# Optimization experiments

Hardware: AMD Instinct MI355X
Metric: run time of the kernel (lower is better)

The kernel has to match this reference:

```python
import jax, jax.numpy as jnp
import numpy as np

INPUT_SIZE = 512
HIDDEN_SIZE = 1024
BATCH = 16384


def setup_inputs() -> dict:
    key = jax.random.key(0)
    ks = jax.random.split(key, 11)
    s_x = 1.0 / np.sqrt(INPUT_SIZE)
    s_h = 1.0 / np.sqrt(HIDDEN_SIZE)
    inp = {
        "x": jax.random.normal(ks[0], (BATCH, INPUT_SIZE), dtype=jnp.float32),
        "hidden": jax.random.normal(ks[1], (BATCH, HIDDEN_SIZE), dtype=jnp.float32),
        # Linear weights stored as (in, out) for x @ W
        "Wxr": jax.random.uniform(ks[2], (INPUT_SIZE, HIDDEN_SIZE), jnp.float32, -s_x, s_x),
        "bxr": jax.random.uniform(ks[3], (HIDDEN_SIZE,), jnp.float32, -s_x, s_x),
        "Whr": jax.random.uniform(ks[4], (HIDDEN_SIZE, HIDDEN_SIZE), jnp.float32, -s_h, s_h),
        "Wxz": jax.random.uniform(ks[5], (INPUT_SIZE, HIDDEN_SIZE), jnp.float32, -s_x, s_x),
        "bxz": jax.random.uniform(ks[6], (HIDDEN_SIZE,), jnp.float32, -s_x, s_x),
        "Whz": jax.random.uniform(ks[7], (HIDDEN_SIZE, HIDDEN_SIZE), jnp.float32, -s_h, s_h),
        "Wxh": jax.random.uniform(ks[8], (INPUT_SIZE, HIDDEN_SIZE), jnp.float32, -s_x, s_x),
        "bxh": jax.random.uniform(ks[9], (HIDDEN_SIZE,), jnp.float32, -s_x, s_x),
        "Whh": jax.random.uniform(ks[10], (HIDDEN_SIZE, HIDDEN_SIZE), jnp.float32, -s_h, s_h),
    }
    return inp


def reference(x, hidden, Wxr, bxr, Whr, Wxz, bxz, Whz, Wxh, bxh, Whh):
    # GRU cell, single timestep.
    r = jax.nn.sigmoid(x @ Wxr + bxr + hidden @ Whr)          # reset gate (B,H)
    z = jax.nn.sigmoid(x @ Wxz + bxz + hidden @ Whz)          # update gate (B,H)
    h_cand = jnp.tanh(x @ Wxh + bxh + (r * hidden) @ Whh)     # candidate (B,H)
    return z * hidden + (1.0 - z) * h_cand
```

## Files before the change

### kernel.cpp

```cpp
#include <hip/hip_runtime.h>

typedef unsigned short u16;
typedef unsigned int u32;
typedef __bf16 bf16x8 __attribute__((ext_vector_type(8)));
typedef float f32x4 __attribute__((ext_vector_type(4)));

#define B_ROWS 16384
#define K1 1536

__device__ __forceinline__ u16 f2bf(float f) {
  u32 u = __float_as_uint(f);
  u = (u + 0x7fffu + ((u >> 16) & 1u)) >> 16;
  return (u16)u;
}
__device__ __forceinline__ float bf2f(u16 b) {
  return __uint_as_float(((u32)b) << 16);
}
__device__ __forceinline__ void gload_lds16(const void* g, void* l) {
  __builtin_amdgcn_global_load_lds((const __attribute__((address_space(1))) void*)g,
                                   (__attribute__((address_space(3))) void*)l,
                                   16, 0, 0);
}

__global__ void prep(const float* __restrict__ x, const float* __restrict__ h,
                     u16* __restrict__ xh,
                     const float* __restrict__ Wxr, const float* __restrict__ Whr,
                     const float* __restrict__ Wxz, const float* __restrict__ Whz,
                     const float* __restrict__ Wxh, const float* __restrict__ Whh,
                     u16* __restrict__ W1t, u16* __restrict__ W2t) {
  if (blockIdx.x < 24576) {
    const int iv = blockIdx.x * 256 + threadIdx.x;
    const int row = iv / 384;
    const int col = (iv - row * 384) * 4;
    const float* src = (col < 512) ? x + (size_t)row * 512 + col
                                   : h + (size_t)row * 1024 + (col - 512);
    float4 v = *(const float4*)src;
    u32 a = (u32)f2bf(v.x) | ((u32)f2bf(v.y) << 16);
    u32 b = (u32)f2bf(v.z) | ((u32)f2bf(v.w) << 16);
    *(uint2*)(xh + (size_t)row * 1536 + col) = make_uint2(a, b);
    return;
  }
  __shared__ float tile[32][33];
  const int idx2 = blockIdx.x - 24576;
  const int z = idx2 >> 10;
  const int rem = idx2 & 1023;
  const int by = rem >> 5, bx = rem & 31;
  const float* W;
  u16* T;
  int Ks, koff, roff;
  switch (z) {
    case 0:  W = Wxr; T = W1t; Ks = 512;  koff = 0;   roff = 0;    break;
    case 1:  W = Whr; T = W1t; Ks = 1024; koff = 512; roff = 0;    break;
    case 2:  W = Wxz; T = W1t; Ks = 512;  koff = 0;   roff = 1024; break;
    case 3:  W = Whz; T = W1t; Ks = 1024; koff = 512; roff = 1024; break;
    case 4:  W = Wxh; T = W2t; Ks = 512;  koff = 0;   roff = 0;    break;
    default: W = Whh; T = W2t; Ks = 1024; koff = 512; roff = 0;    break;
  }
  if (by * 32 >= Ks) return;
  const int tx = threadIdx.x & 31, ty = threadIdx.x >> 5;
#pragma unroll
  for (int r = 0; r < 32; r += 8)
    tile[ty + r][tx] = W[(size_t)(by * 32 + ty + r) * 1024 + bx * 32 + tx];
  __syncthreads();
#pragma unroll
  for (int r = 0; r < 32; r += 8)
    T[(size_t)(roff + bx * 32 + ty + r) * K1 + koff + by * 32 + tx] = f2bf(tile[tx][ty + r]);
}

struct Src {
  const u16 *A, *B;
  u32 sA, sB;
};

__device__ __forceinline__ void gemm256(const Src& S, int nt, int brow, int bcol,
                                        u16* AsU, u16* BsU, f32x4 acc[8][4]) {
  const int tid = threadIdx.x;
  const int l = tid & 63;
  const int wid = tid >> 6;
  const int wr = wid >> 2, wc = wid & 3;
  const int lr = l & 15, kq = l >> 4;
  const int swzB = (lr & 7) * 16;
  const int kswzE = ((tid & 7) ^ ((tid >> 3) & 7)) * 8;
  const int r = tid >> 3;
  char* AsB = (char*)AsU;
  char* BsB = (char*)BsU;
  const int ldsQ = wid << 10;
  const int colK0 = (kq * 16) ^ swzB;
  const int colK1 = (64 + kq * 16) ^ swzB;
  int aRow[8], bRow[4];
#pragma unroll
  for (int m = 0; m < 8; ++m) aRow[m] = (wr * 128 + m * 16 + lr) * 128;
#pragma unroll
  for (int n = 0; n < 4; ++n) bRow[n] = (wc * 64 + n * 16 + lr) * 128;

  u32 offA[4], offB[4];
#pragma unroll
  for (int q = 0; q < 4; ++q) {
    offA[q] = (u32)((brow + q * 64 + r) * S.sA + kswzE) * 2u;
    offB[q] = (u32)((bcol + q * 64 + r) * S.sB + kswzE) * 2u;
  }

#define STG_A01(q_, c_) gload_lds16((const char*)S.A + offA[q_], \
    AsB + (c_) * 32768 + (q_) * 8192 + ldsQ)
#define STG_A23(q_, c_) gload_lds16((const char*)S.A + offA[q_], \
    AsB + (c_) * 32768 + 16384 + ((q_) - 2) * 8192 + ldsQ)
#define STG_B(q_, c_)   gload_lds16((const char*)S.B + offB[q_], \
    BsB + (c_) * 32768 + ((q_) >> 1) * 16384 + ((q_) & 1) * 8192 + ldsQ)

  STG_A01(0, 0); STG_A01(1, 0);
  STG_A23(2, 0); STG_A23(3, 0);
  STG_B(0, 0); STG_B(1, 0); STG_B(2, 0); STG_B(3, 0);
  offA[0] += 128; offA[1] += 128;
  STG_A01(0, 1); STG_A01(1, 1);
  offA[0] += 128; offA[1] += 128;
  offA[2] += 128; offA[3] += 128;
  offB[0] += 128; offB[1] += 128; offB[2] += 128; offB[3] += 128;
  asm volatile("s_waitcnt vmcnt(2)" ::: "memory");
  __builtin_amdgcn_s_barrier();
  asm volatile("" ::: "memory");

  for (int t = 0; t < nt; ++t) {
    const int c = t & 1;
    const int cb = c << 15;
    bf16x8 a[4][2], b[4][2];
#pragma unroll
    for (int m = 0; m < 4; ++m) {
      a[m][0] = *(const bf16x8*)(AsB + cb + aRow[m] + colK0);
      a[m][1] = *(const bf16x8*)(AsB + cb + aRow[m] + colK1);
    }
#pragma unroll
    for (int n = 0; n < 2; ++n) {
      b[n][0] = *(const bf16x8*)(BsB + cb + bRow[n] + colK0);
      b[n][1] = *(const bf16x8*)(BsB + cb + bRow[n] + colK1);
    }
    if (t + 1 < nt) { STG_A23(2, c ^ 1); STG_A23(3, c ^ 1); }
    asm volatile("s_waitcnt lgkmcnt(8)" ::: "memory");
    __builtin_amdgcn_s_barrier();
    asm volatile("s_waitcnt lgkmcnt(0)" ::: "memory");
    __builtin_amdgcn_sched_barrier(0);
    __builtin_amdgcn_s_setprio(1);
#pragma unroll
    for (int kk = 0; kk < 2; ++kk)
#pragma unroll
      for (int m = 0; m < 4; ++m)
#pragma unroll
        for (int n = 0; n < 2; ++n)
          acc[m][n] = __builtin_amdgcn_mfma_f32_16x16x32_bf16(a[m][kk], b[n][kk], acc[m][n], 0, 0, 0);
    __builtin_amdgcn_s_setprio(0);
    __builtin_amdgcn_s_barrier();
    asm volatile("" ::: "memory");
#pragma unroll
    for (int n = 2; n < 4; ++n) {
      b[n][0] = *(const bf16x8*)(BsB + cb + bRow[n] + colK0);
      b[n][1] = *(const bf16x8*)(BsB + cb + bRow[n] + colK1);
    }
    if (t + 1 < nt) { STG_B(0, c ^ 1); STG_B(1, c ^ 1); }
    __builtin_amdgcn_s_barrier();
    asm volatile("s_waitcnt lgkmcnt(0)" ::: "memory");
    __builtin_amdgcn_sched_barrier(0);
    __builtin_amdgcn_s_setprio(1);
#pragma unroll
    for (int kk = 0; kk < 2; ++kk)
#pragma unroll
      for (int m = 0; m < 4; ++m)
#pragma unroll
        for (int n = 2; n < 4; ++n)
          acc[m][n] = __builtin_amdgcn_mfma_f32_16x16x32_bf16(a[m][kk], b[n][kk], acc[m][n], 0, 0, 0);
    __builtin_amdgcn_s_setprio(0);
    __builtin_amdgcn_s_barrier();
    asm volatile("" ::: "memory");
#pragma unroll
    for (int m = 0; m < 4; ++m) {
      a[m][0] = *(const bf16x8*)(AsB + cb + aRow[m + 4] + colK0);
      a[m][1] = *(const bf16x8*)(AsB + cb + aRow[m + 4] + colK1);
    }
    if (t + 1 < nt) { STG_B(2, c ^ 1); STG_B(3, c ^ 1); }
    __builtin_amdgcn_s_barrier();
    asm volatile("s_waitcnt lgkmcnt(0)" ::: "memory");
    __builtin_amdgcn_sched_barrier(0);
    __builtin_amdgcn_s_setprio(1);
#pragma unroll
    for (int kk = 0; kk < 2; ++kk)
#pragma unroll
      for (int m = 0; m < 4; ++m)
#pragma unroll
        for (int n = 2; n < 4; ++n)
          acc[m + 4][n] = __builtin_amdgcn_mfma_f32_16x16x32_bf16(a[m][kk], b[n][kk], acc[m + 4][n], 0, 0, 0);
    __builtin_amdgcn_s_setprio(0);
    __builtin_amdgcn_s_barrier();
    asm volatile("" ::: "memory");
    if (t + 2 < nt) { STG_A01(0, c); STG_A01(1, c); }
    __builtin_amdgcn_s_barrier();
    __builtin_amdgcn_s_setprio(1);
#pragma unroll
    for (int kk = 0; kk < 2; ++kk)
#pragma unroll
      for (int m = 0; m < 4; ++m)
#pragma unroll
        for (int n = 0; n < 2; ++n)
          acc[m + 4][n] = __builtin_amdgcn_mfma_f32_16x16x32_bf16(a[m][kk], b[n][kk], acc[m + 4][n], 0, 0, 0);
    __builtin_amdgcn_s_setprio(0);
    if (t + 2 < nt) { asm volatile("s_waitcnt vmcnt(2)" ::: "memory"); }
    else            { asm volatile("s_waitcnt vmcnt(0)" ::: "memory"); }
    __builtin_amdgcn_s_barrier();
    asm volatile("" ::: "memory");
    offA[0] += 128; offA[1] += 128; offA[2] += 128; offA[3] += 128;
    offB[0] += 128; offB[1] += 128; offB[2] += 128; offB[3] += 128;
  }
#undef STG_A01
#undef STG_A23
#undef STG_B
}

__global__ __launch_bounds__(512, 1) void gru_gemm1(
    const u16* __restrict__ xh, const u16* __restrict__ W1t,
    const float* __restrict__ bxr, const float* __restrict__ bxz,
    u16* __restrict__ rhb, u16* __restrict__ zb) {
  __shared__ __align__(16) u16 As[2 * 256 * 64];
  __shared__ __align__(16) u16 Bs[2 * 256 * 64];
  const int orig = blockIdx.x;
  const int slot = orig >> 3;
  const int mt = (orig & 7) + 8 * (slot >> 3);
  const int jt = slot & 7;
  const int brow = mt * 256;
  const int jcol = jt * 256;

  Src S { xh, W1t, K1, K1 };
  f32x4 acc[8][4] = {};
  gemm256(S, 24, brow, jcol, As, Bs, acc);

  const int l = threadIdx.x & 63;
  const int wid = threadIdx.x >> 6;
  const int wr = wid >> 2, wc = wid & 3;
  const int colb = jcol + wc * 64 + (l & 15);
  const int rowb = brow + wr * 128 + (l >> 4) * 4;
  if (jt < 4) {
#pragma unroll
    for (int n = 0; n < 4; ++n) {
      const int col = colb + n * 16;
      const float bias = bxr[col];
#pragma unroll
      for (int m = 0; m < 8; ++m)
#pragma unroll
        for (int j = 0; j < 4; ++j) {
          const int row = rowb + m * 16 + j;
          const float rg = 1.f / (1.f + __expf(-(acc[m][n][j] + bias)));
          const float hv = bf2f(xh[(size_t)row * K1 + 512 + col]);
          rhb[(size_t)row * 1024 + col] = f2bf(rg * hv);
        }
    }
  } else {
#pragma unroll
    for (int n = 0; n < 4; ++n) {
      const int col = colb + n * 16 - 1024;
      const float bias = bxz[col];
#pragma unroll
      for (int m = 0; m < 8; ++m)
#pragma unroll
        for (int j = 0; j < 4; ++j) {
          const int row = rowb + m * 16 + j;
          const float zg = 1.f / (1.f + __expf(-(acc[m][n][j] + bias)));
          zb[(size_t)row * 1024 + col] = f2bf(zg);
        }
    }
  }
}

__global__ __launch_bounds__(512, 1) void gru_gemm2(
    const u16* __restrict__ xh, const u16* __restrict__ rhb,
    const u16* __restrict__ W2t, const float* __restrict__ bxh,
    const u16* __restrict__ zb, float* __restrict__ out) {
  __shared__ __align__(16) u16 As[2 * 256 * 64];
  __shared__ __align__(16) u16 Bs[2 * 128 * 64];
  const int orig = blockIdx.x;
  const int wg = (orig & 7) * 64 + (orig >> 3);
  const int mt = wg & 63;
  const int jt = wg >> 6;
  const int brow = mt * 256;
  const int jcol = jt * 128;

  const int tid = threadIdx.x;
  const int l = tid & 63;
  const int wid = tid >> 6;
  const int wrk = wid >> 1, wc = wid & 1;
  const int lr = l & 15, kq = l >> 4;
  const int swzB = (lr & 7) * 16;
  const int kswzE = ((tid & 7) ^ ((tid >> 3) & 7)) * 8;
  const int r = tid >> 3;
  char* AsB = (char*)As;
  char* BsB = (char*)Bs;
  const int ldsQ = wid << 10;
  const int colK0 = (kq * 16) ^ swzB;
  const int colK1 = (64 + kq * 16) ^ swzB;
  int aRow[4], bRow[4];
#pragma unroll
  for (int m = 0; m < 4; ++m) aRow[m] = (wrk * 64 + m * 16 + lr) * 128;
#pragma unroll
  for (int n = 0; n < 4; ++n) bRow[n] = (wc * 64 + n * 16 + lr) * 128;

  const u16* pA01 = xh;
  const u16* pA23 = xh;
  u32 offA[4], offB[2];
#pragma unroll
  for (int q = 0; q < 4; ++q) offA[q] = (u32)((brow + q * 64 + r) * K1 + kswzE) * 2u;
#pragma unroll
  for (int q = 0; q < 2; ++q) offB[q] = (u32)((jcol + q * 64 + r) * K1 + kswzE) * 2u;

#define G2_A01(q_, c_) gload_lds16((const char*)pA01 + offA[q_], \
    AsB + (c_) * 32768 + (q_) * 8192 + ldsQ)
#define G2_A23(q_, c_) gload_lds16((const char*)pA23 + offA[q_], \
    AsB + (c_) * 32768 + 16384 + ((q_) - 2) * 8192 + ldsQ)
#define G2_B(q_, c_)   gload_lds16((const char*)W2t + offB[q_], \
    BsB + (c_) * 16384 + (q_) * 8192 + ldsQ)

  G2_A01(0, 0); G2_A01(1, 0);
  G2_A23(2, 0); G2_A23(3, 0);
  G2_B(0, 0); G2_B(1, 0);
  offA[0] += 128; offA[1] += 128;
  G2_A01(0, 1); G2_A01(1, 1);
  offA[0] += 128; offA[1] += 128;
  offA[2] += 128; offA[3] += 128;
  offB[0] += 128; offB[1] += 128;
  asm volatile("s_waitcnt vmcnt(2)" ::: "memory");
  __builtin_amdgcn_s_barrier();
  asm volatile("" ::: "memory");

  f32x4 acc[4][4] = {};
  const int nt = 24;
  for (int t = 0; t < nt; ++t) {
    const int c = t & 1;
    const int cbA = c << 15;
    const int cbB = c << 14;
    bf16x8 a01[2][2], a23[2][2], b01[2][2], b23[2][2];
#pragma unroll
    for (int m = 0; m < 2; ++m) {
      a01[m][0] = *(const bf16x8*)(AsB + cbA + aRow[m] + colK0);
      a01[m][1] = *(const bf16x8*)(AsB + cbA + aRow[m] + colK1);
    }
#pragma unroll
    for (int n = 0; n < 2; ++n) {
      b01[n][0] = *(const bf16x8*)(BsB + cbB + bRow[n] + colK0);
      b01[n][1] = *(const bf16x8*)(BsB + cbB + bRow[n] + colK1);
    }
    if (t + 1 < nt) { G2_A23(2, c ^ 1); G2_A23(3, c ^ 1); }
    __builtin_amdgcn_s_barrier();
    asm volatile("s_waitcnt lgkmcnt(0)" ::: "memory");
    __builtin_amdgcn_sched_barrier(0);
    __builtin_amdgcn_s_setprio(1);
#pragma unroll
    for (int kk = 0; kk < 2; ++kk)
#pragma unroll
      for (int m = 0; m < 2; ++m)
#pragma unroll
        for (int n = 0; n < 2; ++n)
          acc[m][n] = __builtin_amdgcn_mfma_f32_16x16x32_bf16(a01[m][kk], b01[n][kk], acc[m][n], 0, 0, 0);
    __builtin_amdgcn_s_setprio(0);
    __builtin_amdgcn_s_barrier();
    asm volatile("" ::: "memory");
#pragma unroll
    for (int n = 0; n < 2; ++n) {
      b23[n][0] = *(const bf16x8*)(BsB + cbB + bRow[n + 2] + colK0);
      b23[n][1] = *(const bf16x8*)(BsB + cbB + bRow[n + 2] + colK1);
    }
    if (t + 1 < nt) { G2_B(0, c ^ 1); G2_B(1, c ^ 1); }
    __builtin_amdgcn_s_barrier();
    asm volatile("s_waitcnt lgkmcnt(0)" ::: "memory");
    __builtin_amdgcn_sched_barrier(0);
    __builtin_amdgcn_s_setprio(1);
#pragma unroll
    for (int kk = 0; kk < 2; ++kk)
#pragma unroll
      for (int m = 0; m < 2; ++m)
#pragma unroll
        for (int n = 0; n < 2; ++n)
          acc[m][n + 2] = __builtin_amdgcn_mfma_f32_16x16x32_bf16(a01[m][kk], b23[n][kk], acc[m][n + 2], 0, 0, 0);
    __builtin_amdgcn_s_setprio(0);
    __builtin_amdgcn_s_barrier();
    asm volatile("" ::: "memory");
#pragma unroll
    for (int m = 0; m < 2; ++m) {
      a23[m][0] = *(const bf16x8*)(AsB + cbA + aRow[m + 2] + colK0);
      a23[m][1] = *(const bf16x8*)(AsB + cbA + aRow[m + 2] + colK1);
    }
    __builtin_amdgcn_s_barrier();
    asm volatile("s_waitcnt lgkmcnt(0)" ::: "memory");
    __builtin_amdgcn_sched_barrier(0);
    __builtin_amdgcn_s_setprio(1);
#pragma unroll
    for (int kk = 0; kk < 2; ++kk)
#pragma unroll
      for (int m = 0; m < 2; ++m)
#pragma unroll
        for (int n = 0; n < 2; ++n)
          acc[m + 2][n + 2] = __builtin_amdgcn_mfma_f32_16x16x32_bf16(a23[m][kk], b23[n][kk], acc[m + 2][n + 2], 0, 0, 0);
    __builtin_amdgcn_s_setprio(0);
    __builtin_amdgcn_s_barrier();
    asm volatile("" ::: "memory");
    if (t + 2 < nt) { G2_A01(0, c); G2_A01(1, c); }
    __builtin_amdgcn_s_barrier();
    __builtin_amdgcn_s_setprio(1);
#pragma unroll
    for (int kk = 0; kk < 2; ++kk)
#pragma unroll
      for (int m = 0; m < 2; ++m)
#pragma unroll
        for (int n = 0; n < 2; ++n)
          acc[m + 2][n] = __builtin_amdgcn_mfma_f32_16x16x32_bf16(a23[m][kk], b01[n][kk], acc[m + 2][n], 0, 0, 0);
    __builtin_amdgcn_s_setprio(0);
    if (t + 2 < nt) { asm volatile("s_waitcnt vmcnt(2)" ::: "memory"); }
    else            { asm volatile("s_waitcnt vmcnt(0)" ::: "memory"); }
    __builtin_amdgcn_s_barrier();
    asm volatile("" ::: "memory");
    if (t == 5) {
      pA01 = rhb;
      offA[0] = (u32)((brow + 0 * 64 + r) * 1024 + kswzE) * 2u;
      offA[1] = (u32)((brow + 1 * 64 + r) * 1024 + kswzE) * 2u;
    } else { offA[0] += 128; offA[1] += 128; }
    if (t == 6) {
      pA23 = rhb;
      offA[2] = (u32)((brow + 2 * 64 + r) * 1024 + kswzE) * 2u;
      offA[3] = (u32)((brow + 3 * 64 + r) * 1024 + kswzE) * 2u;
    } else { offA[2] += 128; offA[3] += 128; }
    offB[0] += 128; offB[1] += 128;
  }
#undef G2_A01
#undef G2_A23
#undef G2_B

  const int colb = jcol + wc * 64 + (l & 15);
  const int rowb = brow + wrk * 64 + (l >> 4) * 4;
#pragma unroll
  for (int n = 0; n < 4; ++n) {
    const int col = colb + n * 16;
    const float bias = bxh[col];
#pragma unroll
    for (int m = 0; m < 4; ++m)
#pragma unroll
      for (int j = 0; j < 4; ++j) {
        const int row = rowb + m * 16 + j;
        const size_t idx = (size_t)row * 1024 + col;
        const float e = __expf(2.f * (acc[m][n][j] + bias));
        const float hc = 1.f - 2.f / (e + 1.f);
        const float z = bf2f(zb[idx]);
        const float h = bf2f(xh[(size_t)row * K1 + 512 + col]);
        out[idx] = z * h + (1.f - z) * hc;
      }
  }
}

extern "C" void kernel_launch(void* const* d_in, const int* in_sizes, int n_in,
                              void* d_out, int out_size, void* d_ws, size_t ws_size,
                              hipStream_t stream) {
  const float* x      = (const float*)d_in[0];
  const float* hidden = (const float*)d_in[1];
  const float* Wxr = (const float*)d_in[2];
  const float* bxr = (const float*)d_in[3];
  const float* Whr = (const float*)d_in[4];
  const float* Wxz = (const float*)d_in[5];
  const float* bxz = (const float*)d_in[6];
  const float* Whz = (const float*)d_in[7];
  const float* Wxh = (const float*)d_in[8];
  const float* bxh = (const float*)d_in[9];
  const float* Whh = (const float*)d_in[10];
  float* out = (float*)d_out;
  (void)in_sizes; (void)n_in; (void)out_size; (void)ws_size;

  char* p = (char*)d_ws;
  u16* xh  = (u16*)p; p += (size_t)B_ROWS * K1 * 2;
  u16* W1t = (u16*)p; p += (size_t)2048 * K1 * 2;
  u16* W2t = (u16*)p; p += (size_t)1024 * K1 * 2;
  u16* rhb = (u16*)p; p += (size_t)B_ROWS * 1024 * 2;
  u16* zb  = (u16*)p; p += (size_t)B_ROWS * 1024 * 2;

  prep<<<24576 + 6144, 256, 0, stream>>>(x, hidden, xh,
                                         Wxr, Whr, Wxz, Whz, Wxh, Whh, W1t, W2t);
  gru_gemm1<<<512, 512, 0, stream>>>(xh, W1t, bxr, bxz, rhb, zb);
  gru_gemm2<<<512, 512, 0, stream>>>(xh, rhb, W2t, bxh, zb, out);
}
```

Before: 251.5 us.

## Replace gemm1's pipelined 256x256 tile with simple single-buffered 128x128 tiles

Rewrites the first GEMM kernel from a 256x256, 512-thread, double-buffered, finely interleaved pipeline into a 128x128, 256-thread kernel with a single LDS buffer and a K-step of 32. It launches 2048 blocks with two blocks per CU, relying on occupancy rather than explicit prefetch to hide memory latency. The cost is more global traffic per FLOP from the smaller tiles and no overlap of loads with MFMA inside a block. This looks like a simplification or probe that could easily lose to the tuned pipeline.

```diff
diff --git a/kernel.cpp b/kernel.cpp
--- a/kernel.cpp
+++ b/kernel.cpp
@@ -67,180 +67,80 @@
     T[(size_t)(roff + bx * 32 + ty + r) * K1 + koff + by * 32 + tx] = f2bf(tile[tx][ty + r]);
 }
 
-struct Src {
-  const u16 *A, *B;
-  u32 sA, sB;
-};
-
-__device__ __forceinline__ void gemm256(const Src& S, int nt, int brow, int bcol,
-                                        u16* AsU, u16* BsU, f32x4 acc[8][4]) {
+__global__ __launch_bounds__(256, 2) void gru_gemm1(
+    const u16* __restrict__ xh, const u16* __restrict__ W1t,
+    const float* __restrict__ bxr, const float* __restrict__ bxz,
+    u16* __restrict__ rhb, u16* __restrict__ zb) {
+  __shared__ __align__(16) u16 As[128 * 32];
+  __shared__ __align__(16) u16 Bs[128 * 32];
+  const int orig = blockIdx.x;
+  const int slot = orig >> 3;
+  const int jt = slot & 15;
+  const int mt = (orig & 7) + 8 * (slot >> 4);
+  const int brow = mt * 128;
+  const int bcol = jt * 128;
+
   const int tid = threadIdx.x;
   const int l = tid & 63;
   const int wid = tid >> 6;
-  const int wr = wid >> 2, wc = wid & 3;
+  const int wrq = wid >> 1, wcq = wid & 1;
   const int lr = l & 15, kq = l >> 4;
-  const int swzB = (lr & 7) * 16;
-  const int kswzE = ((tid & 7) ^ ((tid >> 3) & 7)) * 8;
-  const int r = tid >> 3;
-  char* AsB = (char*)AsU;
-  char* BsB = (char*)BsU;
-  const int ldsQ = wid << 10;
-  const int colK0 = (kq * 16) ^ swzB;
-  const int colK1 = (64 + kq * 16) ^ swzB;
-  int aRow[8], bRow[4];
-#pragma unroll
-  for (int m = 0; m < 8; ++m) aRow[m] = (wr * 128 + m * 16 + lr) * 128;
-#pragma unroll
-  for (int n = 0; n < 4; ++n) bRow[n] = (wc * 64 + n * 16 + lr) * 128;
-
-  u32 offA[4], offB[4];
-#pragma unroll
-  for (int q = 0; q < 4; ++q) {
-    offA[q] = (u32)((brow + q * 64 + r) * S.sA + kswzE) * 2u;
-    offB[q] = (u32)((bcol + q * 64 + r) * S.sB + kswzE) * 2u;
-  }
-
-#define STG_A01(q_, c_) gload_lds16((const char*)S.A + offA[q_], \
-    AsB + (c_) * 32768 + (q_) * 8192 + ldsQ)
-#define STG_A23(q_, c_) gload_lds16((const char*)S.A + offA[q_], \
-    AsB + (c_) * 32768 + 16384 + ((q_) - 2) * 8192 + ldsQ)
-#define STG_B(q_, c_)   gload_lds16((const char*)S.B + offB[q_], \
-    BsB + (c_) * 32768 + ((q_) >> 1) * 16384 + ((q_) & 1) * 8192 + ldsQ)
-
-  STG_A01(0, 0); STG_A01(1, 0);
-  STG_A23(2, 0); STG_A23(3, 0);
-  STG_B(0, 0); STG_B(1, 0); STG_B(2, 0); STG_B(3, 0);
-  offA[0] += 128; offA[1] += 128;
-  STG_A01(0, 1); STG_A01(1, 1);
-  offA[0] += 128; offA[1] += 128;
-  offA[2] += 128; offA[3] += 128;
-  offB[0] += 128; offB[1] += 128; offB[2] += 128; offB[3] += 128;
-  asm volatile("s_waitcnt vmcnt(2)" ::: "memory");
-  __builtin_amdgcn_s_barrier();
-  asm volatile("" ::: "memory");
-
-  for (int t = 0; t < nt; ++t) {
-    const int c = t & 1;
-    const int cb = c << 15;
-    bf16x8 a[4][2], b[4][2];
-#pragma unroll
-    for (int m = 0; m < 4; ++m) {
-      a[m][0] = *(const bf16x8*)(AsB + cb + aRow[m] + colK0);
-      a[m][1] = *(const bf16x8*)(AsB + cb + aRow[m] + colK1);
-    }
-#pragma unroll
-    for (int n = 0; n < 2; ++n) {
-      b[n][0] = *(const bf16x8*)(BsB + cb + bRow[n] + colK0);
-      b[n][1] = *(const bf16x8*)(BsB + cb + bRow[n] + colK1);
-    }
-    if (t + 1 < nt) { STG_A23(2, c ^ 1); STG_A23(3, c ^ 1); }
-    asm volatile("s_waitcnt lgkmcnt(8)" ::: "memory");
-    __builtin_amdgcn_s_barrier();
+  const int colK = (kq * 16) ^ ((lr & 3) * 16);
+  const int kswzE = ((tid & 3) ^ ((tid >> 2) & 3)) * 8;
+  const int r = tid >> 2;
+  char* AsB = (char*)As;
+  char* BsB = (char*)Bs;
+  const int ldsW = wid << 10;
+  int aRow[4], bRow[4];
+#pragma unroll
+  for (int m = 0; m < 4; ++m) aRow[m] = (wrq * 64 + m * 16 + lr) * 64;
+#pragma unroll
+  for (int n = 0; n < 4; ++n) bRow[n] = (wcq * 64 + n * 16 + lr) * 64;
+
+  u32 offA[2], offB[2];
+#pragma unroll
+  for (int q = 0; q < 2; ++q) {
+    offA[q] = (u32)((brow + q * 64 + r) * K1 + kswzE) * 2u;
+    offB[q] = (u32)((bcol + q * 64 + r) * K1 + kswzE) * 2u;
+  }
+
+  f32x4 acc[4][4] = {};
+  for (int t = 0; t < 48; ++t) {
+    gload_lds16((const char*)xh + offA[0], AsB + ldsW);
+    gload_lds16((const char*)xh + offA[1], AsB + 4096 + ldsW);
+    gload_lds16((const char*)W1t + offB[0], BsB + ldsW);
+    gload_lds16((const char*)W1t + offB[1], BsB + 4096 + ldsW);
+    asm volatile("s_waitcnt vmcnt(0)" ::: "memory");
+    __builtin_amdgcn_s_barrier();
+    asm volatile("" ::: "memory");
+    bf16x8 a[4], b[4];
+#pragma unroll
+    for (int m = 0; m < 4; ++m) a[m] = *(const bf16x8*)(AsB + aRow[m] + colK);
+#pragma unroll
+    for (int n = 0; n < 4; ++n) b[n] = *(const bf16x8*)(BsB + bRow[n] + colK);
     asm volatile("s_waitcnt lgkmcnt(0)" ::: "memory");
     __builtin_amdgcn_sched_barrier(0);
     __builtin_amdgcn_s_setprio(1);
 #pragma unroll
-    for (int kk = 0; kk < 2; ++kk)
-#pragma unroll
-      for (int m = 0; m < 4; ++m)
-#pragma unroll
-        for (int n = 0; n < 2; ++n)
-          acc[m][n] = __builtin_amdgcn_mfma_f32_16x16x32_bf16(a[m][kk], b[n][kk], acc[m][n], 0, 0, 0);
-    __builtin_amdgcn_s_setprio(0);
-    __builtin_amdgcn_s_barrier();
-    asm volatile("" ::: "memory");
-#pragma unroll
-    for (int n = 2; n < 4; ++n) {
-      b[n][0] = *(const bf16x8*)(BsB + cb + bRow[n] + colK0);
-      b[n][1] = *(const bf16x8*)(BsB + cb + bRow[n] + colK1);
-    }
-    if (t + 1 < nt) { STG_B(0, c ^ 1); STG_B(1, c ^ 1); }
-    __builtin_amdgcn_s_barrier();
-    asm volatile("s_waitcnt lgkmcnt(0)" ::: "memory");
-    __builtin_amdgcn_sched_barrier(0);
-    __builtin_amdgcn_s_setprio(1);
-#pragma unroll
-    for (int kk = 0; kk < 2; ++kk)
-#pragma unroll
-      for (int m = 0; m < 4; ++m)
-#pragma unroll
-        for (int n = 2; n < 4; ++n)
-          acc[m][n] = __builtin_amdgcn_mfma_f32_16x16x32_bf16(a[m][kk], b[n][kk], acc[m][n], 0, 0, 0);
-    __builtin_amdgcn_s_setprio(0);
-    __builtin_amdgcn_s_barrier();
-    asm volatile("" ::: "memory");
-#pragma unroll
-    for (int m = 0; m < 4; ++m) {
-      a[m][0] = *(const bf16x8*)(AsB + cb + aRow[m + 4] + colK0);
-      a[m][1] = *(const bf16x8*)(AsB + cb + aRow[m + 4] + colK1);
-    }
-    if (t + 1 < nt) { STG_B(2, c ^ 1); STG_B(3, c ^ 1); }
-    __builtin_amdgcn_s_barrier();
-    asm volatile("s_waitcnt lgkmcnt(0)" ::: "memory");
-    __builtin_amdgcn_sched_barrier(0);
-    __builtin_amdgcn_s_setprio(1);
-#pragma unroll
-    for (int kk = 0; kk < 2; ++kk)
-#pragma unroll
-      for (int m = 0; m < 4; ++m)
-#pragma unroll
-        for (int n = 2; n < 4; ++n)
-          acc[m + 4][n] = __builtin_amdgcn_mfma_f32_16x16x32_bf16(a[m][kk], b[n][kk], acc[m + 4][n], 0, 0, 0);
-    __builtin_amdgcn_s_setprio(0);
-    __builtin_amdgcn_s_barrier();
-    asm volatile("" ::: "memory");
-    if (t + 2 < nt) { STG_A01(0, c); STG_A01(1, c); }
-    __builtin_amdgcn_s_barrier();
-    __builtin_amdgcn_s_setprio(1);
-#pragma unroll
-    for (int kk = 0; kk < 2; ++kk)
-#pragma unroll
-      for (int m = 0; m < 4; ++m)
-#pragma unroll
-        for (int n = 0; n < 2; ++n)
-          acc[m + 4][n] = __builtin_amdgcn_mfma_f32_16x16x32_bf16(a[m][kk], b[n][kk], acc[m + 4][n], 0, 0, 0);
-    __builtin_amdgcn_s_setprio(0);
-    if (t + 2 < nt) { asm volatile("s_waitcnt vmcnt(2)" ::: "memory"); }
-    else            { asm volatile("s_waitcnt vmcnt(0)" ::: "memory"); }
-    __builtin_amdgcn_s_barrier();
-    asm volatile("" ::: "memory");
-    offA[0] += 128; offA[1] += 128; offA[2] += 128; offA[3] += 128;
-    offB[0] += 128; offB[1] += 128; offB[2] += 128; offB[3] += 128;
-  }
-#undef STG_A01
-#undef STG_A23
-#undef STG_B
-}
-
-__global__ __launch_bounds__(512, 1) void gru_gemm1(
-    const u16* __restrict__ xh, const u16* __restrict__ W1t,
-    const float* __restrict__ bxr, const float* __restrict__ bxz,
-    u16* __restrict__ rhb, u16* __restrict__ zb) {
-  __shared__ __align__(16) u16 As[2 * 256 * 64];
-  __shared__ __align__(16) u16 Bs[2 * 256 * 64];
-  const int orig = blockIdx.x;
-  const int slot = orig >> 3;
-  const int mt = (orig & 7) + 8 * (slot >> 3);
-  const int jt = slot & 7;
-  const int brow = mt * 256;
-  const int jcol = jt * 256;
-
-  Src S { xh, W1t, K1, K1 };
-  f32x4 acc[8][4] = {};
-  gemm256(S, 24, brow, jcol, As, Bs, acc);
-
-  const int l = threadIdx.x & 63;
-  const int wid = threadIdx.x >> 6;
-  const int wr = wid >> 2, wc = wid & 3;
-  const int colb = jcol + wc * 64 + (l & 15);
-  const int rowb = brow + wr * 128 + (l >> 4) * 4;
-  if (jt < 4) {
+    for (int m = 0; m < 4; ++m)
+#pragma unroll
+      for (int n = 0; n < 4; ++n)
+        acc[m][n] = __builtin_amdgcn_mfma_f32_16x16x32_bf16(a[m], b[n], acc[m][n], 0, 0, 0);
+    __builtin_amdgcn_s_setprio(0);
+    __builtin_amdgcn_s_barrier();
+    asm volatile("" ::: "memory");
+    offA[0] += 64; offA[1] += 64; offB[0] += 64; offB[1] += 64;
+  }
+
+  const int colb = (jt & 7) * 128 + wcq * 64 + (l & 15);
+  const int rowb = brow + wrq * 64 + (l >> 4) * 4;
+  if (jt < 8) {
 #pragma unroll
     for (int n = 0; n < 4; ++n) {
       const int col = colb + n * 16;
       const float bias = bxr[col];
 #pragma unroll
-      for (int m = 0; m < 8; ++m)
+      for (int m = 0; m < 4; ++m)
 #pragma unroll
         for (int j = 0; j < 4; ++j) {
           const int row = rowb + m * 16 + j;
@@ -252,10 +152,10 @@
   } else {
 #pragma unroll
     for (int n = 0; n < 4; ++n) {
-      const int col = colb + n * 16 - 1024;
+      const int col = colb + n * 16;
       const float bias = bxz[col];
 #pragma unroll
-      for (int m = 0; m < 8; ++m)
+      for (int m = 0; m < 4; ++m)
 #pragma unroll
         for (int j = 0; j < 4; ++j) {
           const int row = rowb + m * 16 + j;
@@ -474,6 +374,6 @@
 
   prep<<<24576 + 6144, 256, 0, stream>>>(x, hidden, xh,
                                          Wxr, Whr, Wxz, Whz, Wxh, Whh, W1t, W2t);
-  gru_gemm1<<<512, 512, 0, stream>>>(xh, W1t, bxr, bxz, rhb, zb);
+  gru_gemm1<<<2048, 256, 0, stream>>>(xh, W1t, bxr, bxz, rhb, zb);
   gru_gemm2<<<512, 512, 0, stream>>>(xh, rhb, W2t, bxh, zb, out);
 }
```

Measured after the change: 289.5 us. +15.1%, slower.
